# Kernel optimization log

Measured on AMD Instinct MI355X. Metric: run time of the kernel, lower is better.

The kernel has to match this reference:

```python
import jax, jax.numpy as jnp
import numpy as np

N_VARS = 28
HID = 64
BATCH = 32768
BN_EPS = 1e-5


def _lin_init(key, fan_in, shape):
    bound = 1.0 / np.sqrt(fan_in)
    return jax.random.uniform(key, shape, minval=-bound, maxval=bound, dtype=jnp.float32)


def setup_inputs() -> dict:
    key = jax.random.key(0)
    ks = jax.random.split(key, 8)
    n, h = N_VARS, HID
    X = jax.random.normal(ks[0], (BATCH, n), dtype=jnp.float32)
    W_logits = jax.random.uniform(ks[1], (n, n), minval=-0.01, maxval=0.01, dtype=jnp.float32)
    # per-mechanism (grouped) weights, stacked on leading mechanism axis n
    W1 = _lin_init(ks[2], n, (n, h, n)); b1 = _lin_init(ks[3], n, (n, h))
    W2 = _lin_init(ks[4], h, (n, h, h)); b2 = _lin_init(ks[5], h, (n, h))
    W3 = _lin_init(ks[6], h, (n, 1, h)); b3 = _lin_init(ks[7], h, (n, 1))
    gamma1 = jnp.ones((n, h)); beta1 = jnp.zeros((n, h))
    gamma2 = jnp.ones((n, h)); beta2 = jnp.zeros((n, h))
    return {"X": X, "W_logits": W_logits,
            "W1": W1, "b1": b1, "gamma1": gamma1, "beta1": beta1,
            "W2": W2, "b2": b2, "gamma2": gamma2, "beta2": beta2,
            "W3": W3, "b3": b3}


def _bn(x, gamma, beta):
    # x: [n, B, h]; batch stats over B (training-mode BatchNorm1d, biased var)
    m = x.mean(axis=1, keepdims=True)
    v = ((x - m) ** 2).mean(axis=1, keepdims=True)
    return gamma[:, None, :] * (x - m) * jax.lax.rsqrt(v + BN_EPS) + beta[:, None, :]


def reference(X, W_logits, W1, b1, gamma1, beta1, W2, b2, gamma2, beta2, W3, b3):
    n = W_logits.shape[0]
    # adjacency: sigmoid with zeroed diagonal
    W = jax.nn.sigmoid(W_logits) * (1.0 - jnp.eye(n, dtype=W_logits.dtype))
    # fuse the parent mask into the first layer's weights: one grouped GEMM
    # instead of n_vars separate masked matmuls
    W1_eff = W1 * W[:, None, :]                               # [n, h, n]
    h1 = jnp.einsum('bd,nhd->nbh', X, W1_eff) + b1[:, None, :]  # [n, B, h]
    a1 = jax.nn.gelu(_bn(h1, gamma1, beta1), approximate=False)
    h2 = jnp.einsum('nbh,ngh->nbg', a1, W2) + b2[:, None, :]
    a2 = jax.nn.gelu(_bn(h2, gamma2, beta2), approximate=False)
    out = jnp.einsum('nbh,noh->nbo', a2, W3) + b3[:, None, :]   # [n, B, 1]
    X_hat = out[:, :, 0].T                                     # [B, n]
    return (X_hat, W)
```

## Files before the change

### kernel.cpp

```cpp
#include <hip/hip_runtime.h>
#include <hip/hip_bf16.h>
#include <math.h>

typedef float  f4 __attribute__((ext_vector_type(4)));
typedef short  s8 __attribute__((ext_vector_type(8)));
typedef short  s4 __attribute__((ext_vector_type(4)));

#define NV 28
#define NB 32768
#define BN_EPS 1e-5f
#define NSLOT 434

#define SUM2_OFF   0
#define SSQ2_OFF   1792
#define BIAS1_OFF  3584
#define PART_OFF   9472
#define BF_BASE_F  120640
#define W2B_OFF_S  57344
#define XBF_OFF_S  172032
#define H2_BYTE_OFF 2924544ull
#define H2_BYTES    117440512ull

__device__ __forceinline__ float gelu_f(float x) {
    float x2 = x * x;
    float z  = x * __builtin_fmaf(x2, -0.10294324f, -2.3022082f);
    float t  = __builtin_amdgcn_exp2f(z);
    return x * __builtin_amdgcn_rcpf(1.0f + t);
}
__device__ __forceinline__ unsigned short f2bf(float x) {
    unsigned u = __builtin_bit_cast(unsigned, x);
    return (unsigned short)((u + 0x7fffu + ((u >> 16) & 1u)) >> 16);
}
__device__ __forceinline__ float bf2f(short s) {
    return __builtin_bit_cast(float, ((int)(unsigned short)s) << 16);
}
__device__ __forceinline__ float row16_sum(float v) {
    int x;
    x = __builtin_amdgcn_update_dpp(0, __builtin_bit_cast(int, v), 0xB1, 0xF, 0xF, true);
    v += __builtin_bit_cast(float, x);
    x = __builtin_amdgcn_update_dpp(0, __builtin_bit_cast(int, v), 0x4E, 0xF, 0xF, true);
    v += __builtin_bit_cast(float, x);
    x = __builtin_amdgcn_update_dpp(0, __builtin_bit_cast(int, v), 0x124, 0xF, 0xF, true);
    v += __builtin_bit_cast(float, x);
    x = __builtin_amdgcn_update_dpp(0, __builtin_bit_cast(int, v), 0x128, 0xF, 0xF, true);
    v += __builtin_bit_cast(float, x);
    return v;
}
__device__ __forceinline__ float quad4_sum(float v) {
    int x;
    x = __builtin_amdgcn_update_dpp(0, __builtin_bit_cast(int, v), 0xB1, 0xF, 0xF, true);
    v += __builtin_bit_cast(float, x);
    x = __builtin_amdgcn_update_dpp(0, __builtin_bit_cast(int, v), 0x4E, 0xF, 0xF, true);
    v += __builtin_bit_cast(float, x);
    return v;
}

__global__ __launch_bounds__(256) void k_xstats(const float* __restrict__ X,
                                                float* __restrict__ ws) {
    __shared__ float sx[128 * 28];
    const int tid = threadIdx.x;
    const int rowbase = blockIdx.x * 128;
    {
        const f4* src = (const f4*)(X + (size_t)rowbase * 28);
        f4* dst = (f4*)sx;
        for (int i = tid; i < 128 * 28 / 4; i += 256) dst[i] = src[i];
    }
    __syncthreads();
    int* xb = (int*)((short*)(ws + BF_BASE_F) + XBF_OFF_S);
    for (int j = tid; j < 128 * 16; j += 256) {
        int row = j >> 4, cc = j & 15;
        float lo = (2 * cc     < 28) ? sx[row * 28 + 2 * cc]     : 0.0f;
        float hi = (2 * cc + 1 < 28) ? sx[row * 28 + 2 * cc + 1] : 0.0f;
        xb[(size_t)(rowbase + row) * 16 + cc] = (int)f2bf(lo) | ((int)f2bf(hi) << 16);
    }
    for (int s = tid; s < NSLOT; s += 256) {
        float a = 0.0f;
        if (s < 28) {
            for (int r = 0; r < 128; ++r) a += sx[r * 28 + s];
        } else {
            int p = s - 28, d = 0, rem = 28;
            while (p >= rem) { p -= rem; ++d; --rem; }
            int e = d + p;
            for (int r = 0; r < 128; ++r)
                a = __builtin_fmaf(sx[r * 28 + d], sx[r * 28 + e], a);
        }
        ws[PART_OFF + blockIdx.x * NSLOT + s] = a;
    }
}

__global__ __launch_bounds__(256) void k_fold1(const float* __restrict__ Wlog,
                                               const float* __restrict__ W1,
                                               const float* __restrict__ g1,
                                               const float* __restrict__ be1,
                                               const float* __restrict__ W2,
                                               float* __restrict__ ws,
                                               float* __restrict__ out_w) {
    __shared__ float sstat[NSLOT];
    __shared__ float mu[28], wrow[28];
    __shared__ float C[784];
    __shared__ float w1e_s[64 * 28];
    const int n = blockIdx.x, t = threadIdx.x;

    for (int s = t; s < NSLOT; s += 256) {
        float a = 0.0f;
#pragma unroll 16
        for (int p = 0; p < 256; ++p) a += ws[PART_OFF + p * NSLOT + s];
        sstat[s] = a;
    }
    if (t < 64) {
        ws[SUM2_OFF + n * 64 + t] = 0.0f;
        ws[SSQ2_OFF + n * 64 + t] = 0.0f;
    }
    __syncthreads();

    if (t < 28) {
        mu[t] = sstat[t] * (1.0f / 32768.0f);
        float w = 1.0f / (1.0f + expf(-Wlog[n * 28 + t]));
        if (t == n) w = 0.0f;
        wrow[t] = w;
        out_w[n * 28 + t] = w;
    }
    __syncthreads();
    for (int i = t; i < 784; i += 256) {
        int d = i / 28, e = i % 28;
        int lo = d < e ? d : e, hi = d < e ? e : d;
        int idx = 28 + lo * 28 - (lo * (lo - 1)) / 2 + (hi - lo);
        C[i] = sstat[idx] * (1.0f / 32768.0f) - mu[d] * mu[e];
    }
    for (int i = t; i < 1792; i += 256)
        w1e_s[i] = W1[(size_t)n * 1792 + i] * wrow[i % 28];
    __syncthreads();

    const int h = t >> 2, j = t & 3;
    const float* we = &w1e_s[h * 28];
    float var_p = 0.0f, dot_p = 0.0f;
#pragma unroll
    for (int k = 0; k < 7; ++k) {
        int d = 7 * j + k;
        float inner = 0.0f;
#pragma unroll
        for (int e = 0; e < 28; ++e) inner = __builtin_fmaf(C[d * 28 + e], we[e], inner);
        float wd = we[d];
        var_p = __builtin_fmaf(inner, wd, var_p);
        dot_p = __builtin_fmaf(wd, mu[d], dot_p);
    }
    float var  = quad4_sum(var_p);
    float dotm = quad4_sum(dot_p);
    float scale = g1[n * 64 + h] * rsqrtf(fmaxf(var, 0.0f) + BN_EPS);
    if (j == 0)
        ws[BIAS1_OFF + n * 64 + h] = be1[n * 64 + h] - dotm * scale;

    short* bfbase = (short*)(ws + BF_BASE_F);
    {
        short* w1f = bfbase + (size_t)(n * 64 + h) * 32;
        s8 pk;
#pragma unroll
        for (int k = 0; k < 8; ++k) {
            int d = 8 * j + k;
            pk[k] = (short)f2bf(d < 28 ? we[d] * scale : 0.0f);
        }
        *(s8*)&w1f[8 * j] = pk;
    }
    {
        const float* w2src = W2 + (size_t)n * 4096 + t * 16;
        short* w2d = bfbase + W2B_OFF_S + (size_t)n * 4096 + t * 16;
        s8 a, b;
#pragma unroll
        for (int k = 0; k < 8; ++k) a[k] = (short)f2bf(w2src[k]);
#pragma unroll
        for (int k = 0; k < 8; ++k) b[k] = (short)f2bf(w2src[8 + k]);
        *(s8*)&w2d[0] = a;
        *(s8*)&w2d[8] = b;
    }
}

template <bool STORE>
__global__ __launch_bounds__(256, 4) void k_pass1(float* __restrict__ ws,
                                                  short* __restrict__ h2buf) {
    __shared__ __align__(16) short sW1[64 * 40];
    __shared__ __align__(16) short sW2[64 * 72];
    __shared__ __align__(16) short sA1[8 * 16 * 72];
    __shared__ float sP1[4][64], sP2[4][64];

    const int n = blockIdx.x >> 7;
    const int blk = blockIdx.x & 127;
    const int tid = threadIdx.x;
    const int wave = tid >> 6;
    const int lane = tid & 63;
    const int m = lane & 15;
    const int q = lane >> 4;

    const short* bfbase = (const short*)(ws + BF_BASE_F);
    const short* w1g = bfbase + (size_t)n * 64 * 32;
    const short* w2g = bfbase + W2B_OFF_S + (size_t)n * 64 * 64;
    const short* xbf = bfbase + XBF_OFF_S;
    {
        int r = tid >> 2, c = tid & 3;
        *(s8*)&sW1[r * 40 + c * 8] = *(const s8*)&w1g[r * 32 + c * 8];
#pragma unroll
        for (int k = 0; k < 2; ++k) {
            int i2 = tid + k * 256;
            int r2 = i2 >> 3, c2 = i2 & 7;
            *(s8*)&sW2[r2 * 72 + c2 * 8] = *(const s8*)&w2g[r2 * 64 + c2 * 8];
        }
    }
    __syncthreads();

    const float* bias1 = ws + BIAS1_OFF + n * 64;
    short* myA1a = &sA1[(wave * 2 + 0) * 16 * 72];
    short* myA1b = &sA1[(wave * 2 + 1) * 16 * 72];
    float s1[16], s2v[16];
#pragma unroll
    for (int i = 0; i < 16; ++i) { s1[i] = 0.0f; s2v[i] = 0.0f; }

#pragma unroll
    for (int it = 0; it < 2; ++it) {
        const int row0 = blk * 256 + it * 128 + wave * 32;
        s8 xfa = *(const s8*)&xbf[(size_t)(row0 + m) * 32 + 8 * q];
        s8 xfb = *(const s8*)&xbf[(size_t)(row0 + 16 + m) * 32 + 8 * q];

        f4 acc1a[4], acc1b[4];
#pragma unroll
        for (int t = 0; t < 4; ++t) {
            s8 wf = *(const s8*)&sW1[(16 * t + m) * 40 + q * 8];
            acc1a[t] = __builtin_amdgcn_mfma_f32_16x16x32_bf16(wf, xfa, (f4){0.f, 0.f, 0.f, 0.f}, 0, 0, 0);
            acc1b[t] = __builtin_amdgcn_mfma_f32_16x16x32_bf16(wf, xfb, (f4){0.f, 0.f, 0.f, 0.f}, 0, 0, 0);
        }
#pragma unroll
        for (int t = 0; t < 4; ++t) {
            f4 bv = *(const f4*)&bias1[16 * t + 4 * q];
            s4 pa, pb;
#pragma unroll
            for (int r = 0; r < 4; ++r) {
                pa[r] = (short)f2bf(gelu_f(acc1a[t][r] + bv[r]));
                pb[r] = (short)f2bf(gelu_f(acc1b[t][r] + bv[r]));
            }
            *(s4*)&myA1a[m * 72 + 16 * t + 4 * q] = pa;
            *(s4*)&myA1b[m * 72 + 16 * t + 4 * q] = pb;
        }
        s8 af0a = *(const s8*)&myA1a[m * 72 + 8 * q];
        s8 af1a = *(const s8*)&myA1a[m * 72 + 32 + 8 * q];
        s8 af0b = *(const s8*)&myA1b[m * 72 + 8 * q];
        s8 af1b = *(const s8*)&myA1b[m * 72 + 32 + 8 * q];
        short* hpA = STORE ? (h2buf + ((size_t)n * NB + row0 + m) * 64) : nullptr;
        short* hpB = STORE ? (h2buf + ((size_t)n * NB + row0 + 16 + m) * 64) : nullptr;
#pragma unroll
        for (int u = 0; u < 4; ++u) {
            s8 w0 = *(const s8*)&sW2[(16 * u + m) * 72 + 8 * q];
            s8 w1 = *(const s8*)&sW2[(16 * u + m) * 72 + 32 + 8 * q];
            f4 aa = (f4){0.f, 0.f, 0.f, 0.f};
            f4 ab = (f4){0.f, 0.f, 0.f, 0.f};
            aa = __builtin_amdgcn_mfma_f32_16x16x32_bf16(w0, af0a, aa, 0, 0, 0);
            ab = __builtin_amdgcn_mfma_f32_16x16x32_bf16(w0, af0b, ab, 0, 0, 0);
            aa = __builtin_amdgcn_mfma_f32_16x16x32_bf16(w1, af1a, aa, 0, 0, 0);
            ab = __builtin_amdgcn_mfma_f32_16x16x32_bf16(w1, af1b, ab, 0, 0, 0);
            if (STORE) {
                s4 ha, hb;
#pragma unroll
                for (int r = 0; r < 4; ++r) { ha[r] = (short)f2bf(aa[r]); hb[r] = (short)f2bf(ab[r]); }
                *(s4*)&hpA[16 * u + 4 * q] = ha;
                *(s4*)&hpB[16 * u + 4 * q] = hb;
            }
#pragma unroll
            for (int r = 0; r < 4; ++r) {
                s1[u * 4 + r]  += aa[r] + ab[r];
                s2v[u * 4 + r] = __builtin_fmaf(aa[r], aa[r], s2v[u * 4 + r]);
                s2v[u * 4 + r] = __builtin_fmaf(ab[r], ab[r], s2v[u * 4 + r]);
            }
        }
    }
#pragma unroll
    for (int u = 0; u < 4; ++u) {
#pragma unroll
        for (int r = 0; r < 4; ++r) {
            float t1 = row16_sum(s1[u * 4 + r]);
            float t2 = row16_sum(s2v[u * 4 + r]);
            if (m == 0) {
                sP1[wave][16 * u + 4 * q + r] = t1;
                sP2[wave][16 * u + 4 * q + r] = t2;
            }
        }
    }
    __syncthreads();
    if (tid < 64) {
        float a = sP1[0][tid] + sP1[1][tid] + sP1[2][tid] + sP1[3][tid];
        float b = sP2[0][tid] + sP2[1][tid] + sP2[2][tid] + sP2[3][tid];
        atomicAdd(&ws[SUM2_OFF + n * 64 + tid], a);
        atomicAdd(&ws[SSQ2_OFF + n * 64 + tid], b);
    }
}

__global__ __launch_bounds__(256) void k_pass2s(const float* __restrict__ g2,
                                                const float* __restrict__ be2,
                                                const float* __restrict__ W3,
                                                const float* __restrict__ b3,
                                                const float* __restrict__ ws,
                                                const short* __restrict__ h2buf,
                                                float* __restrict__ out) {
    __shared__ float sSc[64], sSh[64], sW3v[64];
    const int n = blockIdx.x >> 7;
    const int row = ((blockIdx.x & 127) << 8) + threadIdx.x;
    if (threadIdx.x < 64) {
        int g = threadIdx.x;
        float mean = ws[SUM2_OFF + n * 64 + g] * (1.0f / 32768.0f);
        float var  = ws[SSQ2_OFF + n * 64 + g] * (1.0f / 32768.0f) - mean * mean;
        float sc = g2[n * 64 + g] * rsqrtf(fmaxf(var, 0.0f) + BN_EPS);
        sSc[g]  = sc;
        sSh[g]  = be2[n * 64 + g] - mean * sc;
        sW3v[g] = W3[n * 64 + g];
    }
    __syncthreads();
    const short* hp = h2buf + ((size_t)n * NB + row) * 64;
    float p0 = 0.0f, p1 = 0.0f;
#pragma unroll
    for (int c = 0; c < 8; ++c) {
        s8 hv = *(const s8*)&hp[c * 8];
#pragma unroll
        for (int k = 0; k < 8; ++k) {
            int g = c * 8 + k;
            float v = __builtin_fmaf(bf2f(hv[k]), sSc[g], sSh[g]);
            if (k & 1) p1 = __builtin_fmaf(gelu_f(v), sW3v[g], p1);
            else       p0 = __builtin_fmaf(gelu_f(v), sW3v[g], p0);
        }
    }
    out[(size_t)row * 28 + n] = p0 + p1 + b3[n];
}

__global__ __launch_bounds__(256, 4) void k_pass2r(const float* __restrict__ g2,
                                                   const float* __restrict__ be2,
                                                   const float* __restrict__ W3,
                                                   const float* __restrict__ b3,
                                                   float* __restrict__ ws,
                                                   float* __restrict__ out) {
    __shared__ __align__(16) short sW1[64 * 40];
    __shared__ __align__(16) short sW2[64 * 72];
    __shared__ __align__(16) short sA1[8 * 16 * 72];
    __shared__ float sSc[64], sSh[64], sW3v[64];

    const int n = blockIdx.x >> 7;
    const int blk = blockIdx.x & 127;
    const int tid = threadIdx.x;
    const int wave = tid >> 6;
    const int lane = tid & 63;
    const int m = lane & 15;
    const int q = lane >> 4;

    const short* bfbase = (const short*)(ws + BF_BASE_F);
    const short* w1g = bfbase + (size_t)n * 64 * 32;
    const short* w2g = bfbase + W2B_OFF_S + (size_t)n * 64 * 64;
    const short* xbf = bfbase + XBF_OFF_S;
    {
        int r = tid >> 2, c = tid & 3;
        *(s8*)&sW1[r * 40 + c * 8] = *(const s8*)&w1g[r * 32 + c * 8];
#pragma unroll
        for (int k = 0; k < 2; ++k) {
            int i2 = tid + k * 256;
            int r2 = i2 >> 3, c2 = i2 & 7;
            *(s8*)&sW2[r2 * 72 + c2 * 8] = *(const s8*)&w2g[r2 * 64 + c2 * 8];
        }
        if (tid < 64) {
            float mean = ws[SUM2_OFF + n * 64 + tid] * (1.0f / 32768.0f);
            float var  = ws[SSQ2_OFF + n * 64 + tid] * (1.0f / 32768.0f) - mean * mean;
            float sc = g2[n * 64 + tid] * rsqrtf(fmaxf(var, 0.0f) + BN_EPS);
            sSc[tid]  = sc;
            sSh[tid]  = be2[n * 64 + tid] - mean * sc;
            sW3v[tid] = W3[n * 64 + tid];
        }
    }
    __syncthreads();

    const float* bias1 = ws + BIAS1_OFF + n * 64;
    const float b3n = b3[n];
    short* myA1a = &sA1[(wave * 2 + 0) * 16 * 72];
    short* myA1b = &sA1[(wave * 2 + 1) * 16 * 72];

#pragma unroll
    for (int it = 0; it < 2; ++it) {
        const int row0 = blk * 256 + it * 128 + wave * 32;
        s8 xfa = *(const s8*)&xbf[(size_t)(row0 + m) * 32 + 8 * q];
        s8 xfb = *(const s8*)&xbf[(size_t)(row0 + 16 + m) * 32 + 8 * q];

        f4 acc1a[4], acc1b[4];
#pragma unroll
        for (int t = 0; t < 4; ++t) {
            s8 wf = *(const s8*)&sW1[(16 * t + m) * 40 + q * 8];
            acc1a[t] = __builtin_amdgcn_mfma_f32_16x16x32_bf16(wf, xfa, (f4){0.f, 0.f, 0.f, 0.f}, 0, 0, 0);
            acc1b[t] = __builtin_amdgcn_mfma_f32_16x16x32_bf16(wf, xfb, (f4){0.f, 0.f, 0.f, 0.f}, 0, 0, 0);
        }
#pragma unroll
        for (int t = 0; t < 4; ++t) {
            f4 bv = *(const f4*)&bias1[16 * t + 4 * q];
            s4 pa, pb;
#pragma unroll
            for (int r = 0; r < 4; ++r) {
                pa[r] = (short)f2bf(gelu_f(acc1a[t][r] + bv[r]));
                pb[r] = (short)f2bf(gelu_f(acc1b[t][r] + bv[r]));
            }
            *(s4*)&myA1a[m * 72 + 16 * t + 4 * q] = pa;
            *(s4*)&myA1b[m * 72 + 16 * t + 4 * q] = pb;
        }
        s8 af0a = *(const s8*)&myA1a[m * 72 + 8 * q];
        s8 af1a = *(const s8*)&myA1a[m * 72 + 32 + 8 * q];
        s8 af0b = *(const s8*)&myA1b[m * 72 + 8 * q];
        s8 af1b = *(const s8*)&myA1b[m * 72 + 32 + 8 * q];
        float pa = 0.0f, pb = 0.0f;
#pragma unroll
        for (int u = 0; u < 4; ++u) {
            s8 w0 = *(const s8*)&sW2[(16 * u + m) * 72 + 8 * q];
            s8 w1 = *(const s8*)&sW2[(16 * u + m) * 72 + 32 + 8 * q];
            f4 aa = (f4){0.f, 0.f, 0.f, 0.f};
            f4 ab = (f4){0.f, 0.f, 0.f, 0.f};
            aa = __builtin_amdgcn_mfma_f32_16x16x32_bf16(w0, af0a, aa, 0, 0, 0);
            ab = __builtin_amdgcn_mfma_f32_16x16x32_bf16(w0, af0b, ab, 0, 0, 0);
            aa = __builtin_amdgcn_mfma_f32_16x16x32_bf16(w1, af1a, aa, 0, 0, 0);
            ab = __builtin_amdgcn_mfma_f32_16x16x32_bf16(w1, af1b, ab, 0, 0, 0);
            f4 scv = *(const f4*)&sSc[16 * u + 4 * q];
            f4 shv = *(const f4*)&sSh[16 * u + 4 * q];
            f4 w3v = *(const f4*)&sW3v[16 * u + 4 * q];
#pragma unroll
            for (int r = 0; r < 4; ++r) {
                float va = __builtin_fmaf(aa[r], scv[r], shv[r]);
                float vb = __builtin_fmaf(ab[r], scv[r], shv[r]);
                pa = __builtin_fmaf(gelu_f(va), w3v[r], pa);
                pb = __builtin_fmaf(gelu_f(vb), w3v[r], pb);
            }
        }
        pa += __shfl_xor(pa, 16);  pa += __shfl_xor(pa, 32);
        pb += __shfl_xor(pb, 16);  pb += __shfl_xor(pb, 32);
        if (q == 0) {
            out[(size_t)(row0 + m) * 28 + n]      = pa + b3n;
            out[(size_t)(row0 + 16 + m) * 28 + n] = pb + b3n;
        }
    }
}

extern "C" void kernel_launch(void* const* d_in, const int* in_sizes, int n_in,
                              void* d_out, int out_size, void* d_ws, size_t ws_size,
                              hipStream_t stream) {
    const float* X   = (const float*)d_in[0];
    const float* Wl  = (const float*)d_in[1];
    const float* W1  = (const float*)d_in[2];
    const float* g1  = (const float*)d_in[4];
    const float* be1 = (const float*)d_in[5];
    const float* W2  = (const float*)d_in[6];
    const float* g2  = (const float*)d_in[8];
    const float* be2 = (const float*)d_in[9];
    const float* W3  = (const float*)d_in[10];
    const float* b3  = (const float*)d_in[11];
    float* out = (float*)d_out;
    float* ws  = (float*)d_ws;
    short* h2buf = (short*)((char*)d_ws + H2_BYTE_OFF);
    const bool store_h2 = ws_size >= H2_BYTE_OFF + H2_BYTES;

    k_xstats<<<dim3(256), dim3(256), 0, stream>>>(X, ws);
    k_fold1<<<dim3(28), dim3(256), 0, stream>>>(Wl, W1, g1, be1, W2, ws, out + 917504);
    if (store_h2) {
        k_pass1<true><<<dim3(28 * 128), dim3(256), 0, stream>>>(ws, h2buf);
        k_pass2s<<<dim3(28 * 128), dim3(256), 0, stream>>>(g2, be2, W3, b3, ws, h2buf, out);
    } else {
        k_pass1<false><<<dim3(28 * 128), dim3(256), 0, stream>>>(ws, nullptr);
        k_pass2r<<<dim3(28 * 128), dim3(256), 0, stream>>>(g2, be2, W3, b3, ws, out);
    }
}
```

Baseline: 191.4 us.

## Coalesce h2 reads in pass2 with 8-lane row split and faster bf16 packing

```diff
diff --git a/kernel.cpp b/kernel.cpp
--- a/kernel.cpp
+++ b/kernel.cpp
@@ -5,6 +5,7 @@
 typedef float  f4 __attribute__((ext_vector_type(4)));
 typedef short  s8 __attribute__((ext_vector_type(8)));
 typedef short  s4 __attribute__((ext_vector_type(4)));
+typedef int    i2 __attribute__((ext_vector_type(2)));
 
 #define NV 28
 #define NB 32768
@@ -33,6 +34,11 @@
 }
 __device__ __forceinline__ float bf2f(short s) {
     return __builtin_bit_cast(float, ((int)(unsigned short)s) << 16);
+}
+__device__ __forceinline__ int bfpack(float a, float b) {
+    unsigned ua = __builtin_bit_cast(unsigned, a) + 0x8000u;
+    unsigned ub = __builtin_bit_cast(unsigned, b) + 0x8000u;
+    return __builtin_amdgcn_perm(ub, ua, 0x07060302);
 }
 __device__ __forceinline__ float row16_sum(float v) {
     int x;
@@ -199,14 +205,18 @@
         *(s8*)&sW1[r * 40 + c * 8] = *(const s8*)&w1g[r * 32 + c * 8];
 #pragma unroll
         for (int k = 0; k < 2; ++k) {
-            int i2 = tid + k * 256;
-            int r2 = i2 >> 3, c2 = i2 & 7;
+            int i2x = tid + k * 256;
+            int r2 = i2x >> 3, c2 = i2x & 7;
             *(s8*)&sW2[r2 * 72 + c2 * 8] = *(const s8*)&w2g[r2 * 64 + c2 * 8];
         }
     }
     __syncthreads();
 
     const float* bias1 = ws + BIAS1_OFF + n * 64;
+    f4 biasv[4];
+#pragma unroll
+    for (int t = 0; t < 4; ++t) biasv[t] = *(const f4*)&bias1[16 * t + 4 * q];
+
     short* myA1a = &sA1[(wave * 2 + 0) * 16 * 72];
     short* myA1b = &sA1[(wave * 2 + 1) * 16 * 72];
     float s1[16], s2v[16];
@@ -228,15 +238,18 @@
         }
 #pragma unroll
         for (int t = 0; t < 4; ++t) {
-            f4 bv = *(const f4*)&bias1[16 * t + 4 * q];
-            s4 pa, pb;
-#pragma unroll
-            for (int r = 0; r < 4; ++r) {
-                pa[r] = (short)f2bf(gelu_f(acc1a[t][r] + bv[r]));
-                pb[r] = (short)f2bf(gelu_f(acc1b[t][r] + bv[r]));
-            }
-            *(s4*)&myA1a[m * 72 + 16 * t + 4 * q] = pa;
-            *(s4*)&myA1b[m * 72 + 16 * t + 4 * q] = pb;
+            float ga0 = gelu_f(acc1a[t][0] + biasv[t][0]);
+            float ga1 = gelu_f(acc1a[t][1] + biasv[t][1]);
+            float ga2 = gelu_f(acc1a[t][2] + biasv[t][2]);
+            float ga3 = gelu_f(acc1a[t][3] + biasv[t][3]);
+            float gb0 = gelu_f(acc1b[t][0] + biasv[t][0]);
+            float gb1 = gelu_f(acc1b[t][1] + biasv[t][1]);
+            float gb2 = gelu_f(acc1b[t][2] + biasv[t][2]);
+            float gb3 = gelu_f(acc1b[t][3] + biasv[t][3]);
+            i2 pa = (i2){bfpack(ga0, ga1), bfpack(ga2, ga3)};
+            i2 pb = (i2){bfpack(gb0, gb1), bfpack(gb2, gb3)};
+            *(i2*)&myA1a[m * 72 + 16 * t + 4 * q] = pa;
+            *(i2*)&myA1b[m * 72 + 16 * t + 4 * q] = pb;
         }
         s8 af0a = *(const s8*)&myA1a[m * 72 + 8 * q];
         s8 af1a = *(const s8*)&myA1a[m * 72 + 32 + 8 * q];
@@ -255,11 +268,10 @@
             aa = __builtin_amdgcn_mfma_f32_16x16x32_bf16(w1, af1a, aa, 0, 0, 0);
             ab = __builtin_amdgcn_mfma_f32_16x16x32_bf16(w1, af1b, ab, 0, 0, 0);
             if (STORE) {
-                s4 ha, hb;
-#pragma unroll
-                for (int r = 0; r < 4; ++r) { ha[r] = (short)f2bf(aa[r]); hb[r] = (short)f2bf(ab[r]); }
-                *(s4*)&hpA[16 * u + 4 * q] = ha;
-                *(s4*)&hpB[16 * u + 4 * q] = hb;
+                i2 ha = (i2){bfpack(aa[0], aa[1]), bfpack(aa[2], aa[3])};
+                i2 hb = (i2){bfpack(ab[0], ab[1]), bfpack(ab[2], ab[3])};
+                *(i2*)&hpA[16 * u + 4 * q] = ha;
+                *(i2*)&hpB[16 * u + 4 * q] = hb;
             }
 #pragma unroll
             for (int r = 0; r < 4; ++r) {
@@ -290,7 +302,7 @@
     }
 }
 
-__global__ __launch_bounds__(256) void k_pass2s(const float* __restrict__ g2,
+__global__ __launch_bounds__(256) void k_pass2c(const float* __restrict__ g2,
                                                 const float* __restrict__ be2,
                                                 const float* __restrict__ W3,
                                                 const float* __restrict__ b3,
@@ -298,32 +310,46 @@
                                                 const short* __restrict__ h2buf,
                                                 float* __restrict__ out) {
     __shared__ float sSc[64], sSh[64], sW3v[64];
-    const int n = blockIdx.x >> 7;
-    const int row = ((blockIdx.x & 127) << 8) + threadIdx.x;
-    if (threadIdx.x < 64) {
-        int g = threadIdx.x;
-        float mean = ws[SUM2_OFF + n * 64 + g] * (1.0f / 32768.0f);
-        float var  = ws[SSQ2_OFF + n * 64 + g] * (1.0f / 32768.0f) - mean * mean;
-        float sc = g2[n * 64 + g] * rsqrtf(fmaxf(var, 0.0f) + BN_EPS);
-        sSc[g]  = sc;
-        sSh[g]  = be2[n * 64 + g] - mean * sc;
-        sW3v[g] = W3[n * 64 + g];
-    }
-    __syncthreads();
-    const short* hp = h2buf + ((size_t)n * NB + row) * 64;
-    float p0 = 0.0f, p1 = 0.0f;
-#pragma unroll
-    for (int c = 0; c < 8; ++c) {
-        s8 hv = *(const s8*)&hp[c * 8];
-#pragma unroll
-        for (int k = 0; k < 8; ++k) {
-            int g = c * 8 + k;
-            float v = __builtin_fmaf(bf2f(hv[k]), sSc[g], sSh[g]);
-            if (k & 1) p1 = __builtin_fmaf(gelu_f(v), sW3v[g], p1);
-            else       p0 = __builtin_fmaf(gelu_f(v), sW3v[g], p0);
-        }
-    }
-    out[(size_t)row * 28 + n] = p0 + p1 + b3[n];
+    const int n = blockIdx.x >> 8;
+    const int rbase = (blockIdx.x & 255) * 128;
+    const int tid = threadIdx.x;
+    if (tid < 64) {
+        float mean = ws[SUM2_OFF + n * 64 + tid] * (1.0f / 32768.0f);
+        float var  = ws[SSQ2_OFF + n * 64 + tid] * (1.0f / 32768.0f) - mean * mean;
+        float sc = g2[n * 64 + tid] * rsqrtf(fmaxf(var, 0.0f) + BN_EPS);
+        sSc[tid]  = sc;
+        sSh[tid]  = be2[n * 64 + tid] - mean * sc;
+        sW3v[tid] = W3[n * 64 + tid];
+    }
+    __syncthreads();
+    const int wave = tid >> 6;
+    const int lane = tid & 63;
+    const int rr = lane >> 3;
+    const int cc = lane & 7;
+    f4 scA = *(const f4*)&sSc[cc * 8],     scB = *(const f4*)&sSc[cc * 8 + 4];
+    f4 shA = *(const f4*)&sSh[cc * 8],     shB = *(const f4*)&sSh[cc * 8 + 4];
+    f4 w3A = *(const f4*)&sW3v[cc * 8],    w3B = *(const f4*)&sW3v[cc * 8 + 4];
+    const float b3n = b3[n];
+#pragma unroll
+    for (int it = 0; it < 4; ++it) {
+        const int row = rbase + wave * 32 + it * 8 + rr;
+        s8 hv = *(const s8*)(h2buf + ((size_t)n * NB + row) * 64 + cc * 8);
+        float p = 0.0f;
+#pragma unroll
+        for (int j = 0; j < 4; ++j) {
+            float v = __builtin_fmaf(bf2f(hv[j]), scA[j], shA[j]);
+            p = __builtin_fmaf(gelu_f(v), w3A[j], p);
+        }
+#pragma unroll
+        for (int j = 0; j < 4; ++j) {
+            float v = __builtin_fmaf(bf2f(hv[4 + j]), scB[j], shB[j]);
+            p = __builtin_fmaf(gelu_f(v), w3B[j], p);
+        }
+        p += __shfl_xor(p, 1);
+        p += __shfl_xor(p, 2);
+        p += __shfl_xor(p, 4);
+        if (cc == 0) out[(size_t)row * 28 + n] = p + b3n;
+    }
 }
 
 __global__ __launch_bounds__(256, 4) void k_pass2r(const float* __restrict__ g2,
@@ -354,8 +380,8 @@
         *(s8*)&sW1[r * 40 + c * 8] = *(const s8*)&w1g[r * 32 + c * 8];
 #pragma unroll
         for (int k = 0; k < 2; ++k) {
-            int i2 = tid + k * 256;
-            int r2 = i2 >> 3, c2 = i2 & 7;
+            int i2x = tid + k * 256;
+            int r2 = i2x >> 3, c2 = i2x & 7;
             *(s8*)&sW2[r2 * 72 + c2 * 8] = *(const s8*)&w2g[r2 * 64 + c2 * 8];
         }
         if (tid < 64) {
@@ -456,7 +482,7 @@
     k_fold1<<<dim3(28), dim3(256), 0, stream>>>(Wl, W1, g1, be1, W2, ws, out + 917504);
     if (store_h2) {
         k_pass1<true><<<dim3(28 * 128), dim3(256), 0, stream>>>(ws, h2buf);
-        k_pass2s<<<dim3(28 * 128), dim3(256), 0, stream>>>(g2, be2, W3, b3, ws, h2buf, out);
+        k_pass2c<<<dim3(28 * 256), dim3(256), 0, stream>>>(g2, be2, W3, b3, ws, h2buf, out);
     } else {
         k_pass1<false><<<dim3(28 * 128), dim3(256), 0, stream>>>(ws, nullptr);
         k_pass2r<<<dim3(28 * 128), dim3(256), 0, stream>>>(g2, be2, W3, b3, ws, out);
```

Measured after the change: 173.6 us (median of 2 runs). -9.3%, faster.
